# Kernel tuning notes

Measured on AMD Instinct MI355X. Metric: run time of the kernel, lower is better.

The kernel has to match this reference:

```python
import jax, jax.numpy as jnp
import numpy as np

N = 100000      # nodes
E = 1600000     # edges
D_IN = 256
D_HID = 256
D_OUT = 256
DROP_P = 0.5


def setup_inputs() -> dict:
    key = jax.random.key(0)
    ks = jax.random.split(key, 10)
    s = 1.0 / np.sqrt(D_HID)
    return {
        "z": jax.random.normal(ks[0], (N, D_OUT), jnp.float32),
        "omega": jax.random.normal(ks[1], (N, D_IN), jnp.float32),
        "edge_index": jax.random.randint(ks[2], (2, E), 0, N, jnp.int32),
        "W_lin": jax.random.normal(ks[3], (D_IN, D_HID), jnp.float32) * s,
        "b_lin": jnp.zeros((D_HID,), jnp.float32),
        "W_g1": jax.random.normal(ks[4], (D_HID, D_HID), jnp.float32) * s,
        "b_g1": jnp.zeros((D_HID,), jnp.float32),
        "W_g2": jax.random.normal(ks[5], (D_HID, D_OUT), jnp.float32) * s,
        "b_g2": jnp.zeros((D_OUT,), jnp.float32),
        "mask1": jax.random.bernoulli(ks[6], 1.0 - DROP_P, (N, D_HID)),
        "mask2": jax.random.bernoulli(ks[7], 1.0 - DROP_P, (N, D_HID)),
    }


def _gcn_norm(edge_index):
    # add self-loops, symmetric normalization deg^-1/2 * deg^-1/2
    loop = jnp.arange(N, dtype=edge_index.dtype)
    src = jnp.concatenate([edge_index[0], loop])
    dst = jnp.concatenate([edge_index[1], loop])
    deg = jax.ops.segment_sum(jnp.ones_like(dst, jnp.float32), dst, num_segments=N)
    dinv = jax.lax.rsqrt(deg)  # deg >= 1 because of self-loops
    norm = dinv[src] * dinv[dst]  # [E+N]
    return src, dst, norm


def _gcn_conv(x, W, b, src, dst, norm):
    h = x @ W                                  # [N, d_out]
    msg = h[src] * norm[:, None]               # gather over edges
    out = jax.ops.segment_sum(msg, dst, num_segments=N)  # scatter-add
    return out + b


def _dropout(x, mask):
    return jnp.where(mask, x * (1.0 / (1.0 - DROP_P)), 0.0)


def reference(z, omega, edge_index, W_lin, b_lin, W_g1, b_g1, W_g2, b_g2, mask1, mask2):
    src, dst, norm = _gcn_norm(edge_index)
    # layer 0: Linear + relu + dropout
    h = _dropout(jax.nn.relu(omega @ W_lin + b_lin), mask1)
    # layer 1: GCNConv + relu + dropout
    h = _dropout(jax.nn.relu(_gcn_conv(h, W_g1, b_g1, src, dst, norm)), mask2)
    # layer 2: GCNConv
    h = _gcn_conv(h, W_g2, b_g2, src, dst, norm)
    return z * h
```

## Files before the change

kernel.cpp:

```cpp
#include <hip/hip_runtime.h>
#include <stdint.h>

#define NN 100000
#define EE 1600000
#define DD 256

typedef __bf16 bf16;
typedef __attribute__((ext_vector_type(8))) __bf16 bf16x8;
typedef __attribute__((ext_vector_type(4))) float f32x4;
typedef __attribute__((ext_vector_type(4))) unsigned int u32x4;
typedef __attribute__((ext_vector_type(8))) unsigned short u16x8;

typedef __attribute__((address_space(1))) const unsigned int g_u32c;
typedef __attribute__((address_space(3))) unsigned int lds_u32;

__device__ __forceinline__ float bflo(unsigned int u) {
    union { unsigned int u; float f; } x; x.u = u << 16; return x.f;
}
__device__ __forceinline__ float bfhi(unsigned int u) {
    union { unsigned int u; float f; } x; x.u = u & 0xFFFF0000u; return x.f;
}
__device__ __forceinline__ unsigned short f2bf(float f) {
    return __builtin_bit_cast(unsigned short, (__bf16)f);
}

__global__ void count_deg_k(const int* __restrict__ dst, int* __restrict__ cnt) {
    int e = blockIdx.x * 256 + threadIdx.x;
    if (e < EE) atomicAdd(&cnt[__builtin_nontemporal_load(dst + e)], 1);
}
__global__ __launch_bounds__(256) void scan_blk_k(const int* __restrict__ cnt,
                                                  int* __restrict__ part,
                                                  int* __restrict__ bsum,
                                                  float* __restrict__ dinv) {
    __shared__ int buf[256];
    int i = blockIdx.x * 256 + threadIdx.x;
    int v = 0;
    if (i < NN) { v = cnt[i] + 1; dinv[i] = rsqrtf((float)v); }
    buf[threadIdx.x] = v;
    __syncthreads();
    for (int off = 1; off < 256; off <<= 1) {
        int t = (threadIdx.x >= off) ? buf[threadIdx.x - off] : 0;
        __syncthreads();
        buf[threadIdx.x] += t;
        __syncthreads();
    }
    if (i < NN) part[i] = buf[threadIdx.x];
    if (threadIdx.x == 255) bsum[blockIdx.x] = buf[255];
}
__global__ __launch_bounds__(512) void scan_top_k(const int* __restrict__ bsum,
                                                  int* __restrict__ bpre, int nb) {
    __shared__ int buf[512];
    int v = (threadIdx.x < (unsigned)nb) ? bsum[threadIdx.x] : 0;
    buf[threadIdx.x] = v;
    __syncthreads();
    for (int off = 1; off < 512; off <<= 1) {
        int t = (threadIdx.x >= off) ? buf[threadIdx.x - off] : 0;
        __syncthreads();
        buf[threadIdx.x] += t;
        __syncthreads();
    }
    if (threadIdx.x < (unsigned)nb) bpre[threadIdx.x] = buf[threadIdx.x] - v;
}
__global__ void scan_fin_k(const int* __restrict__ part, const int* __restrict__ bpre,
                           const int* __restrict__ cnt, const float* __restrict__ dinv,
                           int* __restrict__ offs, int* __restrict__ cur,
                           int* __restrict__ cs, float* __restrict__ cw) {
    int i = blockIdx.x * 256 + threadIdx.x;
    if (i >= NN) return;
    int o1 = part[i] + bpre[blockIdx.x];
    offs[i + 1] = o1;
    if (i == 0) offs[0] = 0;
    int o = o1 - (cnt[i] + 1);
    cs[o] = i;
    float di = dinv[i];
    cw[o] = di * di;
    cur[i] = o + 1;
}
__global__ void fill_csr_k(const int* __restrict__ src, const int* __restrict__ dst,
                           const float* __restrict__ dinv, int* __restrict__ cur,
                           int* __restrict__ cs, float* __restrict__ cw) {
    int e = blockIdx.x * 256 + threadIdx.x;
    if (e >= EE) return;
    int s = __builtin_nontemporal_load(src + e);
    int d = __builtin_nontemporal_load(dst + e);
    int pos = atomicAdd(&cur[d], 1);
    cs[pos] = s;
    cw[pos] = dinv[s] * dinv[d];
}

__global__ __launch_bounds__(256) void prep_k(
    const float* __restrict__ W0, const float* __restrict__ W1, const float* __restrict__ W2,
    bf16* __restrict__ T0, bf16* __restrict__ T1, bf16* __restrict__ T2,
    const unsigned int* __restrict__ m, int* __restrict__ flag) {
    int b = blockIdx.x;
    if (b == 192) {
        if (threadIdx.x < 64) {
            unsigned int v = m[threadIdx.x];
            int bad = (v > 1u && v != 0x3F800000u) ? 1 : 0;
            unsigned long long bl = __ballot(bad);
            if (threadIdx.x == 0) *flag = (bl != 0ull) ? 1 : 0;
        }
        return;
    }
    const float* W = b < 64 ? W0 : (b < 128 ? W1 : W2);
    bf16*       T  = b < 64 ? T0 : (b < 128 ? T1 : T2);
    int bb = b & 63;
    __shared__ float tile[32][33];
    int bx = bb & 7, by = bb >> 3;
    int tx = threadIdx.x & 31, ty = threadIdx.x >> 5;
    #pragma unroll
    for (int r = 0; r < 32; r += 8)
        tile[ty + r][tx] = W[(size_t)(by * 32 + ty + r) * DD + bx * 32 + tx];
    __syncthreads();
    #pragma unroll
    for (int r = 0; r < 32; r += 8)
        T[(size_t)(bx * 32 + ty + r) * DD + by * 32 + tx] = (bf16)tile[tx][ty + r];
}

__global__ void cvt_rows_k(const float* __restrict__ in, unsigned short* __restrict__ out) {
    int i = blockIdx.x * 256 + threadIdx.x;
    float4 v = ((const float4*)in)[i];
    ushort4 o = { f2bf(v.x), f2bf(v.y), f2bf(v.z), f2bf(v.w) };
    ((ushort4*)out)[i] = o;
}

template <int ID, int EPI>
__global__ __launch_bounds__(256) void gemm_k(
    const bf16* __restrict__ A, const bf16* __restrict__ Wt,
    const float* __restrict__ bias, const void* __restrict__ mask,
    const int* __restrict__ flagp, const float* __restrict__ z,
    void* __restrict__ outp) {
    __shared__ __align__(16) bf16 As[128 * 64];
    __shared__ __align__(16) bf16 Bs[128 * 64];

    int bid = blockIdx.x;
    int m   = ((bid >> 4) << 3) | (bid & 7);
    int h   = (bid >> 3) & 1;
    int m0  = m * 128, n0 = h * 128;
    if (m0 >= NN) return;
    int tid = threadIdx.x;
    int wid = tid >> 6, lane = tid & 63;
    int wm = wid >> 1, wn = wid & 1;
    int lr = lane & 15, lk = lane >> 4;

    f32x4 acc[4][4] = {};

    for (int k0 = 0; k0 < DD; k0 += 64) {
        #pragma unroll
        for (int i = 0; i < 4; i++) {
            int f = i * 256 + tid;
            int row = f >> 3;
            int c   = (f & 7) * 8;
            int gr = m0 + row; if (gr > NN - 1) gr = NN - 1;
            __builtin_amdgcn_global_load_lds(
                (g_u32c*)(A + (size_t)gr * DD + k0 + c),
                (lds_u32*)(As + (size_t)f * 8), 16, 0, 0);
            __builtin_amdgcn_global_load_lds(
                (g_u32c*)(Wt + (size_t)(n0 + row) * DD + k0 + c),
                (lds_u32*)(Bs + (size_t)f * 8), 16, 0, 0);
        }
        __syncthreads();
        #pragma unroll
        for (int kk = 0; kk < 2; kk++) {
            bf16x8 af[4], bfr[4];
            #pragma unroll
            for (int mi = 0; mi < 4; mi++)
                af[mi] = *(const bf16x8*)(As + (wm * 64 + mi * 16 + lr) * 64 + kk * 32 + lk * 8);
            #pragma unroll
            for (int ni = 0; ni < 4; ni++)
                bfr[ni] = *(const bf16x8*)(Bs + (wn * 64 + ni * 16 + lr) * 64 + kk * 32 + lk * 8);
            #pragma unroll
            for (int mi = 0; mi < 4; mi++)
                #pragma unroll
                for (int ni = 0; ni < 4; ni++)
                    acc[mi][ni] = __builtin_amdgcn_mfma_f32_16x16x32_bf16(
                        bfr[ni], af[mi], acc[mi][ni], 0, 0, 0);
        }
        __syncthreads();
    }

    int bm = (EPI == 1) ? *flagp : 0;
    #pragma unroll
    for (int mi = 0; mi < 4; mi++) {
        int gr = m0 + wm * 64 + mi * 16 + lr;
        if (gr >= NN) continue;
        #pragma unroll
        for (int ni = 0; ni < 4; ni++) {
            int gc = n0 + wn * 64 + ni * 16 + lk * 4;
            size_t idx = (size_t)gr * DD + gc;
            float4 b4 = *(const float4*)(bias + gc);
            float v0 = acc[mi][ni][0] + b4.x;
            float v1 = acc[mi][ni][1] + b4.y;
            float v2 = acc[mi][ni][2] + b4.z;
            float v3 = acc[mi][ni][3] + b4.w;
            if (EPI == 1) {
                v0 = fmaxf(v0, 0.f); v1 = fmaxf(v1, 0.f);
                v2 = fmaxf(v2, 0.f); v3 = fmaxf(v3, 0.f);
                if (bm) {
                    uchar4 u = *(const uchar4*)((const unsigned char*)mask + idx);
                    v0 *= u.x ? 2.f : 0.f; v1 *= u.y ? 2.f : 0.f;
                    v2 *= u.z ? 2.f : 0.f; v3 *= u.w ? 2.f : 0.f;
                } else {
                    uint4 u = *(const uint4*)((const unsigned int*)mask + idx);
                    v0 *= u.x ? 2.f : 0.f; v1 *= u.y ? 2.f : 0.f;
                    v2 *= u.z ? 2.f : 0.f; v3 *= u.w ? 2.f : 0.f;
                }
                ushort4 o = { f2bf(v0), f2bf(v1), f2bf(v2), f2bf(v3) };
                *(ushort4*)((unsigned short*)outp + idx) = o;
            } else {
                f32x4 zz = __builtin_nontemporal_load((const f32x4*)(z + idx));
                f32x4 o = { v0 * zz.x, v1 * zz.y, v2 * zz.z, v3 * zz.w };
                __builtin_nontemporal_store(o, (f32x4*)((float*)outp + idx));
            }
        }
    }
}

__global__ __launch_bounds__(256) void agg_k(
    const bf16* __restrict__ t, const int* __restrict__ offs,
    const int* __restrict__ cs, const float* __restrict__ cw,
    bf16* __restrict__ out) {
    int node = blockIdx.x * 4 + (threadIdx.x >> 6);
    if (node >= NN) return;
    int lane = threadIdx.x & 63;
    int half = lane >> 5;
    int lc = lane & 31;
    int beg = offs[node], end = offs[node + 1];

    float acc[8] = {};
    const unsigned short* tb = (const unsigned short*)t;
    for (int base = beg; base < end; base += 64) {
        int nume = min(64, end - base);
        int sl = 0; float wl = 0.f;
        if (lane < nume) {
            sl = __builtin_nontemporal_load(cs + base + lane);
            wl = __builtin_nontemporal_load(cw + base + lane);
        }
        int nit = (nume + 1) >> 1;
        for (int j = 0; j < nit; j++) {
            int idx = 2 * j + half;
            int s   = __shfl(sl, idx);
            float w = __shfl(wl, idx);
            u32x4 u = *(const u32x4*)(tb + (size_t)s * DD + lc * 8);
            acc[0] = fmaf(w, bflo(u.x), acc[0]);
            acc[1] = fmaf(w, bfhi(u.x), acc[1]);
            acc[2] = fmaf(w, bflo(u.y), acc[2]);
            acc[3] = fmaf(w, bfhi(u.y), acc[3]);
            acc[4] = fmaf(w, bflo(u.z), acc[4]);
            acc[5] = fmaf(w, bfhi(u.z), acc[5]);
            acc[6] = fmaf(w, bflo(u.w), acc[6]);
            acc[7] = fmaf(w, bfhi(u.w), acc[7]);
        }
    }
    #pragma unroll
    for (int i = 0; i < 8; i++) acc[i] += __shfl_xor(acc[i], 32);
    if (half == 0) {
        u16x8 o = { f2bf(acc[0]), f2bf(acc[1]), f2bf(acc[2]), f2bf(acc[3]),
                    f2bf(acc[4]), f2bf(acc[5]), f2bf(acc[6]), f2bf(acc[7]) };
        __builtin_nontemporal_store(o, (u16x8*)((unsigned short*)out + (size_t)node * DD + lc * 8));
    }
}

extern "C" void kernel_launch(void* const* d_in, const int* in_sizes, int n_in,
                              void* d_out, int out_size, void* d_ws, size_t ws_size,
                              hipStream_t stream) {
    const float* z     = (const float*)d_in[0];
    const float* omega = (const float*)d_in[1];
    const int*   eidx  = (const int*)d_in[2];
    const float* W_lin = (const float*)d_in[3];
    const float* b_lin = (const float*)d_in[4];
    const float* W_g1  = (const float*)d_in[5];
    const float* b_g1  = (const float*)d_in[6];
    const float* W_g2  = (const float*)d_in[7];
    const float* b_g2  = (const float*)d_in[8];
    const void*  mask1 = d_in[9];
    const void*  mask2 = d_in[10];

    const int* e_src = eidx;
    const int* e_dst = eidx + EE;

    char* p = (char*)d_ws;
    size_t off = 0;
    auto alloc = [&](size_t bytes) -> char* {
        char* r = p + off;
        off = (off + bytes + 255) & ~(size_t)255;
        return r;
    };
    const int NB256 = (NN + 255) / 256;
    int*   flag = (int*)  alloc(4);
    int*   cnt  = (int*)  alloc((size_t)NN * 4);
    int*   offs = (int*)  alloc(((size_t)NN + 1) * 4);
    int*   cur  = (int*)  alloc((size_t)NN * 4);
    int*   part = (int*)  alloc((size_t)NN * 4);
    int*   bsum = (int*)  alloc(512 * 4);
    int*   bpre = (int*)  alloc(512 * 4);
    float* dinv = (float*)alloc((size_t)NN * 4);
    int*   cs   = (int*)  alloc((size_t)(EE + NN) * 4);
    float* cw   = (float*)alloc((size_t)(EE + NN) * 4);
    bf16*  WtL  = (bf16*) alloc((size_t)DD * DD * 2);
    bf16*  Wt1  = (bf16*) alloc((size_t)DD * DD * 2);
    bf16*  Wt2  = (bf16*) alloc((size_t)DD * DD * 2);
    const size_t NBH = (size_t)NN * DD * 2;
    bf16*  S1   = (bf16*) alloc(NBH);
    bf16*  S2   = (bf16*) alloc(NBH);
    bf16*  S0   = (bf16*)d_out;

    (void)hipMemsetAsync(cnt, 0, (size_t)NN * 4, stream);
    count_deg_k<<<EE / 256, 256, 0, stream>>>(e_dst, cnt);
    scan_blk_k <<<NB256, 256, 0, stream>>>(cnt, part, bsum, dinv);
    scan_top_k <<<1, 512, 0, stream>>>(bsum, bpre, NB256);
    scan_fin_k <<<NB256, 256, 0, stream>>>(part, bpre, cnt, dinv, offs, cur, cs, cw);
    fill_csr_k <<<EE / 256, 256, 0, stream>>>(e_src, e_dst, dinv, cur, cs, cw);

    prep_k<<<193, 256, 0, stream>>>(W_lin, W_g1, W_g2, WtL, Wt1, Wt2,
                                    (const unsigned int*)mask1, flag);
    cvt_rows_k<<<NN * DD / 4 / 256, 256, 0, stream>>>(omega, (unsigned short*)S0);

    const int GG = 1568;
    gemm_k<0, 1><<<GG, 256, 0, stream>>>(S0, WtL, b_lin, mask1, flag, nullptr, S1);
    agg_k<<<NN / 4, 256, 0, stream>>>(S1, offs, cs, cw, S2);
    gemm_k<1, 1><<<GG, 256, 0, stream>>>(S2, Wt1, b_g1, mask2, flag, nullptr, S1);
    agg_k<<<NN / 4, 256, 0, stream>>>(S1, offs, cs, cw, S2);
    gemm_k<2, 2><<<GG, 256, 0, stream>>>(S2, Wt2, b_g2, nullptr, flag, z, d_out);
}
```

Measured before the change: 655.8 us.

## Factor GCN edge norm into per-node dinv scaling and prefetch rows in aggregation

Removes the per-edge weight array. The source-side deg^-1/2 is folded into the epilogue of the GEMM that feeds the aggregation, and the destination-side factor is applied once per node at the end of agg_k. This drops the cw reads and writes in CSR build and aggregation, along with the dinv gathers in fill_csr_k. The aggregation loop is also software-pipelined to load the next neighbor row before accumulating the current one. The cost is extra registers, and the bf16 rounding point for the scaled values changes slightly.

Result: slower. 669.6 us (+2.1%).

```diff
diff --git a/kernel.cpp b/kernel.cpp
--- a/kernel.cpp
+++ b/kernel.cpp
@@ -62,9 +62,9 @@
     if (threadIdx.x < (unsigned)nb) bpre[threadIdx.x] = buf[threadIdx.x] - v;
 }
 __global__ void scan_fin_k(const int* __restrict__ part, const int* __restrict__ bpre,
-                           const int* __restrict__ cnt, const float* __restrict__ dinv,
+                           const int* __restrict__ cnt,
                            int* __restrict__ offs, int* __restrict__ cur,
-                           int* __restrict__ cs, float* __restrict__ cw) {
+                           int* __restrict__ cs) {
     int i = blockIdx.x * 256 + threadIdx.x;
     if (i >= NN) return;
     int o1 = part[i] + bpre[blockIdx.x];
@@ -72,20 +72,16 @@
     if (i == 0) offs[0] = 0;
     int o = o1 - (cnt[i] + 1);
     cs[o] = i;
-    float di = dinv[i];
-    cw[o] = di * di;
     cur[i] = o + 1;
 }
 __global__ void fill_csr_k(const int* __restrict__ src, const int* __restrict__ dst,
-                           const float* __restrict__ dinv, int* __restrict__ cur,
-                           int* __restrict__ cs, float* __restrict__ cw) {
+                           int* __restrict__ cur, int* __restrict__ cs) {
     int e = blockIdx.x * 256 + threadIdx.x;
     if (e >= EE) return;
     int s = __builtin_nontemporal_load(src + e);
     int d = __builtin_nontemporal_load(dst + e);
     int pos = atomicAdd(&cur[d], 1);
     cs[pos] = s;
-    cw[pos] = dinv[s] * dinv[d];
 }
 
 __global__ __launch_bounds__(256) void prep_k(
@@ -129,7 +125,7 @@
     const bf16* __restrict__ A, const bf16* __restrict__ Wt,
     const float* __restrict__ bias, const void* __restrict__ mask,
     const int* __restrict__ flagp, const float* __restrict__ z,
-    void* __restrict__ outp) {
+    const float* __restrict__ dinv, void* __restrict__ outp) {
     __shared__ __align__(16) bf16 As[128 * 64];
     __shared__ __align__(16) bf16 Bs[128 * 64];
 
@@ -184,6 +180,7 @@
     for (int mi = 0; mi < 4; mi++) {
         int gr = m0 + wm * 64 + mi * 16 + lr;
         if (gr >= NN) continue;
+        float ds = (EPI == 1) ? dinv[gr] : 0.f;
         #pragma unroll
         for (int ni = 0; ni < 4; ni++) {
             int gc = n0 + wn * 64 + ni * 16 + lk * 4;
@@ -205,6 +202,7 @@
                     v0 *= u.x ? 2.f : 0.f; v1 *= u.y ? 2.f : 0.f;
                     v2 *= u.z ? 2.f : 0.f; v3 *= u.w ? 2.f : 0.f;
                 }
+                v0 *= ds; v1 *= ds; v2 *= ds; v3 *= ds;
                 ushort4 o = { f2bf(v0), f2bf(v1), f2bf(v2), f2bf(v3) };
                 *(ushort4*)((unsigned short*)outp + idx) = o;
             } else {
@@ -218,7 +216,7 @@
 
 __global__ __launch_bounds__(256) void agg_k(
     const bf16* __restrict__ t, const int* __restrict__ offs,
-    const int* __restrict__ cs, const float* __restrict__ cw,
+    const int* __restrict__ cs, const float* __restrict__ dinv,
     bf16* __restrict__ out) {
     int node = blockIdx.x * 4 + (threadIdx.x >> 6);
     if (node >= NN) return;
@@ -231,29 +229,37 @@
     const unsigned short* tb = (const unsigned short*)t;
     for (int base = beg; base < end; base += 64) {
         int nume = min(64, end - base);
-        int sl = 0; float wl = 0.f;
-        if (lane < nume) {
-            sl = __builtin_nontemporal_load(cs + base + lane);
-            wl = __builtin_nontemporal_load(cw + base + lane);
-        }
+        int sl = 0;
+        if (lane < nume) sl = __builtin_nontemporal_load(cs + base + lane);
         int nit = (nume + 1) >> 1;
+        int i0 = half;
+        int s0 = __shfl(sl, i0);
+        float m0 = (i0 < nume) ? 1.f : 0.f;
+        u32x4 u0 = *(const u32x4*)(tb + (size_t)s0 * DD + lc * 8);
         for (int j = 0; j < nit; j++) {
-            int idx = 2 * j + half;
-            int s   = __shfl(sl, idx);
-            float w = __shfl(wl, idx);
-            u32x4 u = *(const u32x4*)(tb + (size_t)s * DD + lc * 8);
-            acc[0] = fmaf(w, bflo(u.x), acc[0]);
-            acc[1] = fmaf(w, bfhi(u.x), acc[1]);
-            acc[2] = fmaf(w, bflo(u.y), acc[2]);
-            acc[3] = fmaf(w, bfhi(u.y), acc[3]);
-            acc[4] = fmaf(w, bflo(u.z), acc[4]);
-            acc[5] = fmaf(w, bfhi(u.z), acc[5]);
-            acc[6] = fmaf(w, bflo(u.w), acc[6]);
-            acc[7] = fmaf(w, bfhi(u.w), acc[7]);
-        }
-    }
+            int i1 = 2 * (j + 1) + half;
+            int s1 = __shfl(sl, i1 & 63);
+            float m1 = (i1 < nume) ? 1.f : 0.f;
+            u32x4 u1;
+            if (j + 1 < nit)
+                u1 = *(const u32x4*)(tb + (size_t)s1 * DD + lc * 8);
+            acc[0] = fmaf(m0, bflo(u0.x), acc[0]);
+            acc[1] = fmaf(m0, bfhi(u0.x), acc[1]);
+            acc[2] = fmaf(m0, bflo(u0.y), acc[2]);
+            acc[3] = fmaf(m0, bfhi(u0.y), acc[3]);
+            acc[4] = fmaf(m0, bflo(u0.z), acc[4]);
+            acc[5] = fmaf(m0, bfhi(u0.z), acc[5]);
+            acc[6] = fmaf(m0, bflo(u0.w), acc[6]);
+            acc[7] = fmaf(m0, bfhi(u0.w), acc[7]);
+            u0 = u1; m0 = m1;
+        }
+    }
+    float dn = dinv[node];
     #pragma unroll
-    for (int i = 0; i < 8; i++) acc[i] += __shfl_xor(acc[i], 32);
+    for (int i = 0; i < 8; i++) {
+        acc[i] += __shfl_xor(acc[i], 32);
+        acc[i] *= dn;
+    }
     if (half == 0) {
         u16x8 o = { f2bf(acc[0]), f2bf(acc[1]), f2bf(acc[2]), f2bf(acc[3]),
                     f2bf(acc[4]), f2bf(acc[5]), f2bf(acc[6]), f2bf(acc[7]) };
@@ -296,7 +302,6 @@
     int*   bpre = (int*)  alloc(512 * 4);
     float* dinv = (float*)alloc((size_t)NN * 4);
     int*   cs   = (int*)  alloc((size_t)(EE + NN) * 4);
-    float* cw   = (float*)alloc((size_t)(EE + NN) * 4);
     bf16*  WtL  = (bf16*) alloc((size_t)DD * DD * 2);
     bf16*  Wt1  = (bf16*) alloc((size_t)DD * DD * 2);
     bf16*  Wt2  = (bf16*) alloc((size_t)DD * DD * 2);
@@ -309,17 +314,17 @@
     count_deg_k<<<EE / 256, 256, 0, stream>>>(e_dst, cnt);
     scan_blk_k <<<NB256, 256, 0, stream>>>(cnt, part, bsum, dinv);
     scan_top_k <<<1, 512, 0, stream>>>(bsum, bpre, NB256);
-    scan_fin_k <<<NB256, 256, 0, stream>>>(part, bpre, cnt, dinv, offs, cur, cs, cw);
-    fill_csr_k <<<EE / 256, 256, 0, stream>>>(e_src, e_dst, dinv, cur, cs, cw);
+    scan_fin_k <<<NB256, 256, 0, stream>>>(part, bpre, cnt, offs, cur, cs);
+    fill_csr_k <<<EE / 256, 256, 0, stream>>>(e_src, e_dst, cur, cs);
 
     prep_k<<<193, 256, 0, stream>>>(W_lin, W_g1, W_g2, WtL, Wt1, Wt2,
                                     (const unsigned int*)mask1, flag);
     cvt_rows_k<<<NN * DD / 4 / 256, 256, 0, stream>>>(omega, (unsigned short*)S0);
 
     const int GG = 1568;
-    gemm_k<0, 1><<<GG, 256, 0, stream>>>(S0, WtL, b_lin, mask1, flag, nullptr, S1);
-    agg_k<<<NN / 4, 256, 0, stream>>>(S1, offs, cs, cw, S2);
-    gemm_k<1, 1><<<GG, 256, 0, stream>>>(S2, Wt1, b_g1, mask2, flag, nullptr, S1);
-    agg_k<<<NN / 4, 256, 0, stream>>>(S1, offs, cs, cw, S2);
-    gemm_k<2, 2><<<GG, 256, 0, stream>>>(S2, Wt2, b_g2, nullptr, flag, z, d_out);
-}
+    gemm_k<0, 1><<<GG, 256, 0, stream>>>(S0, WtL, b_lin, mask1, flag, nullptr, dinv, S1);
+    agg_k<<<NN / 4, 256, 0, stream>>>(S1, offs, cs, dinv, S2);
+    gemm_k<1, 1><<<GG, 256, 0, stream>>>(S2, Wt1, b_g1, mask2, flag, nullptr, dinv, S1);
+    agg_k<<<NN / 4, 256, 0, stream>>>(S1, offs, cs, dinv, S2);
+    gemm_k<2, 2><<<GG, 256, 0, stream>>>(S2, Wt2, b_g2, nullptr, flag, z, dinv, d_out);
+}
```
